# Kernel optimization log

Measured on AMD Instinct MI355X. Metric: run time of the kernel, lower is better.

## Reference

```python
import jax, jax.numpy as jnp
import numpy as np

C = 256
CK = C // 8  # qk projection dim


def setup_inputs() -> dict:
    key = jax.random.key(0)
    ks = jax.random.split(key, 8)
    B, H, W = 4, 64, 64
    x = jax.random.normal(ks[0], (B, C, W, H), dtype=jnp.float32)
    s = 1.0 / np.sqrt(C)
    Wf = jax.random.normal(ks[1], (CK, C), dtype=jnp.float32) * s
    bf = jax.random.normal(ks[2], (CK,), dtype=jnp.float32) * 0.01
    Wg = jax.random.normal(ks[3], (CK, C), dtype=jnp.float32) * s
    bg = jax.random.normal(ks[4], (CK,), dtype=jnp.float32) * 0.01
    Wh = jax.random.normal(ks[5], (C, C), dtype=jnp.float32) * s
    bh = jax.random.normal(ks[6], (C,), dtype=jnp.float32) * 0.01
    gamma = jax.random.normal(ks[7], (1,), dtype=jnp.float32) * 0.1
    return {"x": x, "Wf": Wf, "bf": bf, "Wg": Wg, "bg": bg,
            "Wh": Wh, "bh": bh, "gamma": gamma}


def reference(x, Wf, bf, Wg, bg, Wh, bh, gamma):
    B, Cc, Wd, Hd = x.shape
    N = Wd * Hd
    xf = x.reshape(B, Cc, N)  # B C N
    # 1x1 conv1d == channel matmul
    f = jnp.einsum('oc,bcn->bon', Wf, xf) + bf[None, :, None]  # B CK N
    g = jnp.einsum('oc,bcn->bon', Wg, xf) + bg[None, :, None]  # B CK N
    h = jnp.einsum('oc,bcn->bon', Wh, xf) + bh[None, :, None]  # B C N
    # s[b,i,j] = sum_k f[b,k,i] g[b,k,j]
    s = jnp.einsum('bki,bkj->bij', f, g)  # B N N
    attention = jax.nn.softmax(s, axis=-1)
    # out[b,c,i] = sum_j h[b,c,j] attention[b,i,j]
    out = jnp.einsum('bcj,bij->bci', h, attention)  # B C N
    out = out.reshape(B, Cc, Wd, Hd)
    return gamma[0] * out + x
```

## Files before the change

### kernel.cpp

```cpp
#include <hip/hip_runtime.h>

typedef __bf16 bf16x8 __attribute__((ext_vector_type(8)));
typedef __bf16 bf16x4 __attribute__((ext_vector_type(4)));
typedef float f32x4 __attribute__((ext_vector_type(4)));
typedef float f32x16 __attribute__((ext_vector_type(16)));

__device__ __forceinline__ f32x4 mfma16(bf16x8 a, bf16x8 b, f32x4 c) {
  return __builtin_amdgcn_mfma_f32_16x16x32_bf16(a, b, c, 0, 0, 0);
}
__device__ __forceinline__ f32x16 mfma32(bf16x8 a, bf16x8 b, f32x16 c) {
  return __builtin_amdgcn_mfma_f32_32x32x16_bf16(a, b, c, 0, 0, 0);
}

__device__ __forceinline__ unsigned int cvtpk(float a, float b) {
  union { __bf16 h[2]; unsigned int u; } r;
  r.h[0] = (__bf16)a; r.h[1] = (__bf16)b;
  return r.u;
}
__device__ __forceinline__ void swap32(unsigned int &a, unsigned int &b) {
  asm("v_permlane32_swap_b32 %0, %1" : "+v"(a), "+v"(b));
}

__global__ void wcvt_kernel(const float* __restrict__ Wf, const float* __restrict__ Wg,
                            const float* __restrict__ Wh, __bf16* __restrict__ Wb) {
  int i = blockIdx.x * 256 + threadIdx.x;
  float v;
  if (i < 8192)       v = Wf[i];
  else if (i < 16384) v = Wg[i - 8192];
  else                v = Wh[i - 16384];
  Wb[i] = (__bf16)v;
}

__global__ __launch_bounds__(512) void proj_kernel(
    const float* __restrict__ x, const float* __restrict__ bfv,
    const float* __restrict__ bgv, const float* __restrict__ bhv,
    const __bf16* __restrict__ Wb, __bf16* __restrict__ qkpk,
    __bf16* __restrict__ vpk) {
  __shared__ __align__(16) char smem[2560 + 18432];
  __bf16* xT = (__bf16*)smem;
  __bf16* ho = (__bf16*)(smem + 2560);

  const int t = threadIdx.x;
  const int l = t & 63, wg = t >> 6, q = l >> 4, l15 = l & 15;
  const int nh = wg & 1, oh = wg >> 1;
  const int bi = blockIdx.x;
  const int b = bi >> 7;
  const int nt = bi & 127;
  const int n0 = nt << 5;

  const float* xb = x + (size_t)b * 256 * 4096;

  f32x4 acc[5];
#pragma unroll
  for (int i = 0; i < 5; i++) acc[i] = (f32x4){0.f, 0.f, 0.f, 0.f};

  const int c_rel = t >> 4;
  const int n2 = (t & 15) * 2;

#pragma unroll 1
  for (int kc = 0; kc < 8; kc++) {
    __syncthreads();
    float2 v = *(const float2*)(xb + (size_t)(kc * 32 + c_rel) * 4096 + n0 + n2);
    xT[(n2 + 0) * 40 + c_rel] = (__bf16)v.x;
    xT[(n2 + 1) * 40 + c_rel] = (__bf16)v.y;
    __syncthreads();
    bf16x8 af = *(const bf16x8*)(xT + (nh * 16 + l15) * 40 + q * 8);
    const __bf16* wp = Wb + (size_t)(oh * 80 + l15) * 256 + kc * 32 + q * 8;
#pragma unroll
    for (int ot = 0; ot < 5; ot++) {
      bf16x8 bfr = *(const bf16x8*)(wp + (size_t)ot * 16 * 256);
      acc[ot] = mfma16(af, bfr, acc[ot]);
    }
  }

#pragma unroll
  for (int ot = 0; ot < 5; ot++) {
    int o = oh * 80 + ot * 16 + l15;
    float bias = (o < 32) ? bfv[o] : (o < 64) ? bgv[o - 32] : bhv[o - 64];
    if (oh == 0 && ot < 4) {
      int qk = o >> 5, fr = (o >> 4) & 1, hh = (o >> 3) & 1, e = o & 7;
      size_t base = ((size_t)b * 128 + nt) * 2048 + qk * 1024 + fr * 512 + hh * 256;
#pragma unroll
      for (int r = 0; r < 4; r++) {
        int n_rel = nh * 16 + q * 4 + r;
        qkpk[base + n_rel * 8 + e] = (__bf16)(acc[ot][r] + bias);
      }
    } else {
#pragma unroll
      for (int r = 0; r < 4; r++) {
        int n_rel = nh * 16 + q * 4 + r;
        ho[(o - 64) * 36 + n_rel] = (__bf16)(acc[ot][r] + bias);
      }
    }
  }
  __syncthreads();
  unsigned short* vpku = (unsigned short*)vpk + (size_t)b * 1048576;
  const unsigned short* hou = (const unsigned short*)ho;
  for (int e = t; e < 4096; e += 512) {
    int c = e >> 4, nn = (e & 15) * 2;
    int n = n0 + nn;
    int jc = n >> 4, hh = (n >> 3) & 1, ee = n & 7;
    unsigned int vv = *(const unsigned int*)(hou + c * 36 + nn);
    *(unsigned int*)(vpku + (((size_t)(jc * 2 + hh) * 256 + c) * 8 + ee)) = vv;
  }
}

__global__ __launch_bounds__(512, 2) void attn_kernel(
    const __bf16* __restrict__ qkpk, const __bf16* __restrict__ vpk,
    __bf16* __restrict__ pO, float* __restrict__ Lp) {
  __shared__ __align__(16) char smem[139264];

  const int t = threadIdx.x;
  const int l = t & 63, w = t >> 6;
  const int h = l >> 5, l31 = l & 31;

  const int bi = blockIdx.x;
  const int xcd = bi & 7;
  const int combo = xcd * 2 + ((bi >> 3) & 1);
  const int ig = bi >> 4;
  const int b = combo >> 2, jp = combo & 3;
  const int ti = ig * 8 + w;
  const int n0 = ti << 5;

  const __bf16* qkb = qkpk + (size_t)b * 262144;
  const __bf16* vpb = vpk + (size_t)b * 1048576;
  const int jq0 = jp << 10;

  const __bf16* qp = qkb + (size_t)ti * 2048 + h * 256 + l31 * 8;
  const bf16x8 qf0 = *(const bf16x8*)(qp);
  const bf16x8 qf1 = *(const bf16x8*)(qp + 512);

  f32x16 acc[8] = {};
  float rsum = 0.f;

  const __bf16* kbase = qkb + 1024 + h * 256 + l31 * 8;
  const int vlane = h * 2048 + l31 * 8;

  bf16x8 kf0 = *(const bf16x8*)(kbase + (size_t)(jq0 >> 5) * 2048);
  bf16x8 kf1 = *(const bf16x8*)(kbase + (size_t)(jq0 >> 5) * 2048 + 512);

#pragma unroll 1
  for (int ch = 0; ch < 32; ++ch) {
    f32x16 s = {};
    s = mfma32(kf0, qf0, s);
    s = mfma32(kf1, qf1, s);

    if (ch < 31) {
      const __bf16* kp = kbase + (size_t)((jq0 >> 5) + ch + 1) * 2048;
      kf0 = *(const bf16x8*)(kp);
      kf1 = *(const bf16x8*)(kp + 512);
    }

    const __bf16* vchunk = vpb + (size_t)((jq0 >> 4) + ch * 2) * 4096 + vlane;
    bf16x8 vb0[8];
#pragma unroll
    for (int ct = 0; ct < 8; ct++)
      vb0[ct] = *(const bf16x8*)(vchunk + ct * 256);

    float p[16];
#pragma unroll
    for (int r = 0; r < 16; r++) { p[r] = __expf(s[r]); rsum += p[r]; }

    unsigned int u0 = cvtpk(p[0], p[1]), v0 = cvtpk(p[2], p[3]);
    unsigned int w0 = cvtpk(p[4], p[5]), z0 = cvtpk(p[6], p[7]);
    swap32(u0, w0); swap32(v0, z0);
    unsigned int u1 = cvtpk(p[8], p[9]), v1 = cvtpk(p[10], p[11]);
    unsigned int w1 = cvtpk(p[12], p[13]), z1 = cvtpk(p[14], p[15]);
    swap32(u1, w1); swap32(v1, z1);
    union { unsigned int u[4]; bf16x8 v; } A0, A1;
    A0.u[0] = u0; A0.u[1] = v0; A0.u[2] = w0; A0.u[3] = z0;
    A1.u[0] = u1; A1.u[1] = v1; A1.u[2] = w1; A1.u[3] = z1;

    bf16x8 vb1[8];
#pragma unroll
    for (int ct = 0; ct < 8; ct++)
      vb1[ct] = *(const bf16x8*)(vchunk + 4096 + ct * 256);

#pragma unroll
    for (int ct = 0; ct < 8; ct++) acc[ct] = mfma32(A0.v, vb0[ct], acc[ct]);
#pragma unroll
    for (int ct = 0; ct < 8; ct++) acc[ct] = mfma32(A1.v, vb1[ct], acc[ct]);
  }

  __bf16* stage = (__bf16*)smem + (size_t)w * 8704;
#pragma unroll
  for (int ct = 0; ct < 8; ct++) {
    int c0 = ct * 32 + l31;
#pragma unroll
    for (int r = 0; r < 16; r++) {
      int i_loc = (r & 3) + 8 * (r >> 2) + 4 * h;
      stage[c0 * 34 + i_loc] = (__bf16)acc[ct][r];
    }
  }
  asm volatile("s_waitcnt lgkmcnt(0)" ::: "memory");

  unsigned short* ob = (unsigned short*)pO + (size_t)(jp * 4 + b) * 1048576 + n0;
  const unsigned short* su = (const unsigned short*)stage;
#pragma unroll 1
  for (int e = l; e < 4096; e += 64) {
    int c = e >> 4, i2 = (e & 15) * 2;
    unsigned int vv = *(const unsigned int*)(su + c * 34 + i2);
    *(unsigned int*)(ob + (size_t)c * 4096 + i2) = vv;
  }

  rsum += __shfl_xor(rsum, 32);
  if (l < 32) Lp[(size_t)(jp * 4 + b) * 4096 + n0 + l] = rsum;
}

__global__ __launch_bounds__(256) void norm_kernel(
    const float* __restrict__ x, const float* __restrict__ gamma_p,
    const __bf16* __restrict__ pO, const float* __restrict__ Lp,
    float* __restrict__ out) {
  const int bc = blockIdx.x;
  const int b = bc >> 8;
  const float gm = gamma_p[0];
  const float* xr = x + (size_t)bc * 4096;
  float* orow = out + (size_t)bc * 4096;
  const __bf16* pbase = pO + (size_t)bc * 4096;
  const float* lbase = Lp + (size_t)b * 4096;

  for (int i0 = threadIdx.x * 4; i0 < 4096; i0 += 1024) {
    float4 xv = *(const float4*)(xr + i0);
    float s0 = 0.f, s1 = 0.f, s2 = 0.f, s3 = 0.f;
    float l0 = 0.f, l1 = 0.f, l2 = 0.f, l3 = 0.f;
#pragma unroll
    for (int jp = 0; jp < 4; jp++) {
      bf16x4 pv = *(const bf16x4*)(pbase + (size_t)jp * 4194304 + i0);
      s0 += (float)pv[0]; s1 += (float)pv[1]; s2 += (float)pv[2]; s3 += (float)pv[3];
      float4 lv = *(const float4*)(lbase + (size_t)jp * 16384 + i0);
      l0 += lv.x; l1 += lv.y; l2 += lv.z; l3 += lv.w;
    }
    float4 ov;
    ov.x = gm * s0 / l0 + xv.x;
    ov.y = gm * s1 / l1 + xv.y;
    ov.z = gm * s2 / l2 + xv.z;
    ov.w = gm * s3 / l3 + xv.w;
    *(float4*)(orow + i0) = ov;
  }
}

extern "C" void kernel_launch(void* const* d_in, const int* in_sizes, int n_in,
                              void* d_out, int out_size, void* d_ws, size_t ws_size,
                              hipStream_t stream) {
  const float* x   = (const float*)d_in[0];
  const float* Wf  = (const float*)d_in[1];
  const float* bfv = (const float*)d_in[2];
  const float* Wg  = (const float*)d_in[3];
  const float* bgv = (const float*)d_in[4];
  const float* Wh  = (const float*)d_in[5];
  const float* bhv = (const float*)d_in[6];
  const float* gm  = (const float*)d_in[7];
  float* out = (float*)d_out;

  char* ws = (char*)d_ws;
  __bf16* Wb   = (__bf16*)ws;
  __bf16* qkpk = (__bf16*)(ws + 262144);
  __bf16* vpk  = (__bf16*)(ws + 2359296);
  __bf16* pO   = (__bf16*)(ws + 10747904);
  float*  Lp   = (float*)(ws + 44302336);

  hipLaunchKernelGGL(wcvt_kernel, dim3(320), dim3(256), 0, stream, Wf, Wg, Wh, Wb);
  hipLaunchKernelGGL(proj_kernel, dim3(512), dim3(512), 0, stream,
                     x, bfv, bgv, bhv, Wb, qkpk, vpk);
  hipLaunchKernelGGL(attn_kernel, dim3(256), dim3(512), 0, stream,
                     qkpk, vpk, pO, Lp);
  hipLaunchKernelGGL(norm_kernel, dim3(1024), dim3(256), 0, stream,
                     x, gm, pO, Lp, out);
}
```

Before: 162.0 us.

## Stage V chunks through double-buffered LDS shared by all waves

All 8 waves in a block read the same V chunk. Before, each wave loaded those 16 fragments from global memory itself. Now the block loads each chunk cooperatively (two 16-byte loads per thread) one iteration ahead, writes it into a double-buffered LDS region, and every wave reads its fragments from LDS. This cuts redundant global/L2 traffic by about 8x, at the cost of a block-wide barrier every iteration, which can serialize the waves and reduce latency hiding.

```diff
diff --git a/kernel.cpp b/kernel.cpp
--- a/kernel.cpp
+++ b/kernel.cpp
@@ -19,6 +19,11 @@
 }
 __device__ __forceinline__ void swap32(unsigned int &a, unsigned int &b) {
   asm("v_permlane32_swap_b32 %0, %1" : "+v"(a), "+v"(b));
+}
+
+__device__ __forceinline__ void sync_lds() {
+  asm volatile("s_waitcnt lgkmcnt(0)" ::: "memory");
+  __builtin_amdgcn_s_barrier();
 }
 
 __global__ void wcvt_kernel(const float* __restrict__ Wf, const float* __restrict__ Wg,
@@ -109,6 +114,7 @@
     const __bf16* __restrict__ qkpk, const __bf16* __restrict__ vpk,
     __bf16* __restrict__ pO, float* __restrict__ Lp) {
   __shared__ __align__(16) char smem[139264];
+  __bf16* Vbuf = (__bf16*)smem;
 
   const int t = threadIdx.x;
   const int l = t & 63, w = t >> 6;
@@ -134,13 +140,29 @@
   float rsum = 0.f;
 
   const __bf16* kbase = qkb + 1024 + h * 256 + l31 * 8;
-  const int vlane = h * 2048 + l31 * 8;
+  const int vfo = h * 2048 + l31 * 8;
 
   bf16x8 kf0 = *(const bf16x8*)(kbase + (size_t)(jq0 >> 5) * 2048);
   bf16x8 kf1 = *(const bf16x8*)(kbase + (size_t)(jq0 >> 5) * 2048 + 512);
 
+  {
+    const __bf16* src = vpb + (size_t)(jq0 >> 4) * 4096;
+    bf16x8 a = *(const bf16x8*)(src + t * 8);
+    bf16x8 c = *(const bf16x8*)(src + 4096 + t * 8);
+    *(bf16x8*)(Vbuf + t * 8) = a;
+    *(bf16x8*)(Vbuf + 4096 + t * 8) = c;
+  }
+  sync_lds();
+
 #pragma unroll 1
   for (int ch = 0; ch < 32; ++ch) {
+    bf16x8 sv0, sv1;
+    if (ch < 31) {
+      const __bf16* src = vpb + (size_t)((jq0 >> 4) + (ch + 1) * 2) * 4096;
+      sv0 = *(const bf16x8*)(src + t * 8);
+      sv1 = *(const bf16x8*)(src + 4096 + t * 8);
+    }
+
     f32x16 s = {};
     s = mfma32(kf0, qf0, s);
     s = mfma32(kf1, qf1, s);
@@ -150,12 +172,6 @@
       kf0 = *(const bf16x8*)(kp);
       kf1 = *(const bf16x8*)(kp + 512);
     }
-
-    const __bf16* vchunk = vpb + (size_t)((jq0 >> 4) + ch * 2) * 4096 + vlane;
-    bf16x8 vb0[8];
-#pragma unroll
-    for (int ct = 0; ct < 8; ct++)
-      vb0[ct] = *(const bf16x8*)(vchunk + ct * 256);
 
     float p[16];
 #pragma unroll
@@ -171,15 +187,24 @@
     A0.u[0] = u0; A0.u[1] = v0; A0.u[2] = w0; A0.u[3] = z0;
     A1.u[0] = u1; A1.u[1] = v1; A1.u[2] = w1; A1.u[3] = z1;
 
-    bf16x8 vb1[8];
-#pragma unroll
-    for (int ct = 0; ct < 8; ct++)
-      vb1[ct] = *(const bf16x8*)(vchunk + 4096 + ct * 256);
-
-#pragma unroll
-    for (int ct = 0; ct < 8; ct++) acc[ct] = mfma32(A0.v, vb0[ct], acc[ct]);
-#pragma unroll
-    for (int ct = 0; ct < 8; ct++) acc[ct] = mfma32(A1.v, vb1[ct], acc[ct]);
+    const __bf16* rb = Vbuf + (ch & 1) * 8192;
+#pragma unroll
+    for (int ct = 0; ct < 8; ct++) {
+      bf16x8 vv = *(const bf16x8*)(rb + vfo + ct * 256);
+      acc[ct] = mfma32(A0.v, vv, acc[ct]);
+    }
+#pragma unroll
+    for (int ct = 0; ct < 8; ct++) {
+      bf16x8 vv = *(const bf16x8*)(rb + 4096 + vfo + ct * 256);
+      acc[ct] = mfma32(A1.v, vv, acc[ct]);
+    }
+
+    if (ch < 31) {
+      __bf16* wb = Vbuf + ((ch + 1) & 1) * 8192;
+      *(bf16x8*)(wb + t * 8) = sv0;
+      *(bf16x8*)(wb + 4096 + t * 8) = sv1;
+    }
+    sync_lds();
   }
 
   __bf16* stage = (__bf16*)smem + (size_t)w * 8704;
```

After: 161.0 us. About the same (-0.6%).

## Split attention work per wave into 64 rows by 128 channels; fold log2e into K

Applied to the files above, without the earlier changes.

Each wave now handles two 32-row query tiles over half of the 256 value channels, where before it handled one query tile over all channels. Each V fragment loaded from global memory is therefore reused by two query tiles, which halves V traffic per unit of work, and V loads are software-pipelined across channel tiles. The K projection is prescaled by log2(e) so the softmax can use exp2 directly. In exchange, each wave now recomputes the QK scores for both tiles (the two channel-half waves duplicate that work), the staging buffer layout changes, and register pressure rises.

```diff
diff --git a/kernel.cpp b/kernel.cpp
--- a/kernel.cpp
+++ b/kernel.cpp
@@ -80,10 +80,11 @@
     if (oh == 0 && ot < 4) {
       int qk = o >> 5, fr = (o >> 4) & 1, hh = (o >> 3) & 1, e = o & 7;
       size_t base = ((size_t)b * 128 + nt) * 2048 + qk * 1024 + fr * 512 + hh * 256;
+      float sc = (o >= 32) ? 1.44269504089f : 1.0f;
 #pragma unroll
       for (int r = 0; r < 4; r++) {
         int n_rel = nh * 16 + q * 4 + r;
-        qkpk[base + n_rel * 8 + e] = (__bf16)(acc[ot][r] + bias);
+        qkpk[base + n_rel * 8 + e] = (__bf16)((acc[ot][r] + bias) * sc);
       }
     } else {
 #pragma unroll
@@ -108,7 +109,7 @@
 __global__ __launch_bounds__(512, 2) void attn_kernel(
     const __bf16* __restrict__ qkpk, const __bf16* __restrict__ vpk,
     __bf16* __restrict__ pO, float* __restrict__ Lp) {
-  __shared__ __align__(16) char smem[139264];
+  __shared__ __align__(16) char smem[135168];
 
   const int t = threadIdx.x;
   const int l = t & 63, w = t >> 6;
@@ -119,92 +120,121 @@
   const int combo = xcd * 2 + ((bi >> 3) & 1);
   const int ig = bi >> 4;
   const int b = combo >> 2, jp = combo & 3;
-  const int ti = ig * 8 + w;
-  const int n0 = ti << 5;
+  const int ih = w >> 1, chalf = w & 1;
+  const int i0 = ig * 256 + ih * 64;
 
   const __bf16* qkb = qkpk + (size_t)b * 262144;
   const __bf16* vpb = vpk + (size_t)b * 1048576;
   const int jq0 = jp << 10;
 
-  const __bf16* qp = qkb + (size_t)ti * 2048 + h * 256 + l31 * 8;
-  const bf16x8 qf0 = *(const bf16x8*)(qp);
-  const bf16x8 qf1 = *(const bf16x8*)(qp + 512);
-
-  f32x16 acc[8] = {};
-  float rsum = 0.f;
+  const __bf16* qpA = qkb + (size_t)(i0 >> 5) * 2048 + h * 256 + l31 * 8;
+  const bf16x8 qA0 = *(const bf16x8*)(qpA);
+  const bf16x8 qA1 = *(const bf16x8*)(qpA + 512);
+  const bf16x8 qB0 = *(const bf16x8*)(qpA + 2048);
+  const bf16x8 qB1 = *(const bf16x8*)(qpA + 2048 + 512);
+
+  f32x16 acc[2][4] = {};
+  float rsA = 0.f, rsB = 0.f;
 
   const __bf16* kbase = qkb + 1024 + h * 256 + l31 * 8;
-  const int vlane = h * 2048 + l31 * 8;
+  const int vfo = h * 2048 + (chalf * 128 + l31) * 8;
 
   bf16x8 kf0 = *(const bf16x8*)(kbase + (size_t)(jq0 >> 5) * 2048);
   bf16x8 kf1 = *(const bf16x8*)(kbase + (size_t)(jq0 >> 5) * 2048 + 512);
 
 #pragma unroll 1
   for (int ch = 0; ch < 32; ++ch) {
+    const __bf16* vchunk = vpb + (size_t)((jq0 >> 4) + ch * 2) * 4096 + vfo;
+    bf16x8 va = *(const bf16x8*)(vchunk);
+    bf16x8 vb_ = *(const bf16x8*)(vchunk + 4096);
+
     f32x16 s = {};
-    s = mfma32(kf0, qf0, s);
-    s = mfma32(kf1, qf1, s);
-
+    s = mfma32(kf0, qA0, s);
+    s = mfma32(kf1, qA1, s);
+    f32x16 sB = {};
+    sB = mfma32(kf0, qB0, sB);
+    sB = mfma32(kf1, qB1, sB);
+
+    bf16x8 kn0, kn1;
     if (ch < 31) {
       const __bf16* kp = kbase + (size_t)((jq0 >> 5) + ch + 1) * 2048;
-      kf0 = *(const bf16x8*)(kp);
-      kf1 = *(const bf16x8*)(kp + 512);
-    }
-
-    const __bf16* vchunk = vpb + (size_t)((jq0 >> 4) + ch * 2) * 4096 + vlane;
-    bf16x8 vb0[8];
-#pragma unroll
-    for (int ct = 0; ct < 8; ct++)
-      vb0[ct] = *(const bf16x8*)(vchunk + ct * 256);
+      kn0 = *(const bf16x8*)(kp);
+      kn1 = *(const bf16x8*)(kp + 512);
+    }
 
     float p[16];
 #pragma unroll
-    for (int r = 0; r < 16; r++) { p[r] = __expf(s[r]); rsum += p[r]; }
-
-    unsigned int u0 = cvtpk(p[0], p[1]), v0 = cvtpk(p[2], p[3]);
-    unsigned int w0 = cvtpk(p[4], p[5]), z0 = cvtpk(p[6], p[7]);
-    swap32(u0, w0); swap32(v0, z0);
-    unsigned int u1 = cvtpk(p[8], p[9]), v1 = cvtpk(p[10], p[11]);
-    unsigned int w1 = cvtpk(p[12], p[13]), z1 = cvtpk(p[14], p[15]);
-    swap32(u1, w1); swap32(v1, z1);
+    for (int r = 0; r < 16; r++) { p[r] = exp2f(s[r]); rsA += p[r]; }
+    unsigned int a0 = cvtpk(p[0], p[1]), a1 = cvtpk(p[2], p[3]);
+    unsigned int a2 = cvtpk(p[4], p[5]), a3 = cvtpk(p[6], p[7]);
+    swap32(a0, a2); swap32(a1, a3);
+    unsigned int a4 = cvtpk(p[8], p[9]), a5 = cvtpk(p[10], p[11]);
+    unsigned int a6 = cvtpk(p[12], p[13]), a7 = cvtpk(p[14], p[15]);
+    swap32(a4, a6); swap32(a5, a7);
     union { unsigned int u[4]; bf16x8 v; } A0, A1;
-    A0.u[0] = u0; A0.u[1] = v0; A0.u[2] = w0; A0.u[3] = z0;
-    A1.u[0] = u1; A1.u[1] = v1; A1.u[2] = w1; A1.u[3] = z1;
-
-    bf16x8 vb1[8];
-#pragma unroll
-    for (int ct = 0; ct < 8; ct++)
-      vb1[ct] = *(const bf16x8*)(vchunk + 4096 + ct * 256);
-
-#pragma unroll
-    for (int ct = 0; ct < 8; ct++) acc[ct] = mfma32(A0.v, vb0[ct], acc[ct]);
-#pragma unroll
-    for (int ct = 0; ct < 8; ct++) acc[ct] = mfma32(A1.v, vb1[ct], acc[ct]);
-  }
-
-  __bf16* stage = (__bf16*)smem + (size_t)w * 8704;
-#pragma unroll
-  for (int ct = 0; ct < 8; ct++) {
-    int c0 = ct * 32 + l31;
-#pragma unroll
-    for (int r = 0; r < 16; r++) {
-      int i_loc = (r & 3) + 8 * (r >> 2) + 4 * h;
-      stage[c0 * 34 + i_loc] = (__bf16)acc[ct][r];
-    }
-  }
+    A0.u[0] = a0; A0.u[1] = a1; A0.u[2] = a2; A0.u[3] = a3;
+    A1.u[0] = a4; A1.u[1] = a5; A1.u[2] = a6; A1.u[3] = a7;
+
+#pragma unroll
+    for (int r = 0; r < 16; r++) { p[r] = exp2f(sB[r]); rsB += p[r]; }
+    unsigned int b0 = cvtpk(p[0], p[1]), b1 = cvtpk(p[2], p[3]);
+    unsigned int b2 = cvtpk(p[4], p[5]), b3 = cvtpk(p[6], p[7]);
+    swap32(b0, b2); swap32(b1, b3);
+    unsigned int b4 = cvtpk(p[8], p[9]), b5 = cvtpk(p[10], p[11]);
+    unsigned int b6 = cvtpk(p[12], p[13]), b7 = cvtpk(p[14], p[15]);
+    swap32(b4, b6); swap32(b5, b7);
+    union { unsigned int u[4]; bf16x8 v; } B0, B1;
+    B0.u[0] = b0; B0.u[1] = b1; B0.u[2] = b2; B0.u[3] = b3;
+    B1.u[0] = b4; B1.u[1] = b5; B1.u[2] = b6; B1.u[3] = b7;
+
+    if (ch < 31) { kf0 = kn0; kf1 = kn1; }
+
+#pragma unroll
+    for (int ct = 0; ct < 4; ct++) {
+      bf16x8 na, nb;
+      if (ct < 3) {
+        na = *(const bf16x8*)(vchunk + (ct + 1) * 256);
+        nb = *(const bf16x8*)(vchunk + 4096 + (ct + 1) * 256);
+      }
+      acc[0][ct] = mfma32(A0.v, va, acc[0][ct]);
+      acc[1][ct] = mfma32(B0.v, va, acc[1][ct]);
+      acc[0][ct] = mfma32(A1.v, vb_, acc[0][ct]);
+      acc[1][ct] = mfma32(B1.v, vb_, acc[1][ct]);
+      if (ct < 3) { va = na; vb_ = nb; }
+    }
+  }
+
+  __bf16* stage = (__bf16*)smem + (size_t)w * 8448;
+#pragma unroll
+  for (int it = 0; it < 2; it++)
+#pragma unroll
+    for (int ct = 0; ct < 4; ct++) {
+      int c0 = ct * 32 + l31;
+#pragma unroll
+      for (int r = 0; r < 16; r++) {
+        int i_loc = it * 32 + (r & 3) + 8 * (r >> 2) + 4 * h;
+        stage[c0 * 66 + i_loc] = (__bf16)acc[it][ct][r];
+      }
+    }
   asm volatile("s_waitcnt lgkmcnt(0)" ::: "memory");
 
-  unsigned short* ob = (unsigned short*)pO + (size_t)(jp * 4 + b) * 1048576 + n0;
+  unsigned short* ob = (unsigned short*)pO + (size_t)(jp * 4 + b) * 1048576 +
+                       (size_t)chalf * 128 * 4096 + i0;
   const unsigned short* su = (const unsigned short*)stage;
 #pragma unroll 1
   for (int e = l; e < 4096; e += 64) {
-    int c = e >> 4, i2 = (e & 15) * 2;
-    unsigned int vv = *(const unsigned int*)(su + c * 34 + i2);
+    int c = e >> 5, i2 = (e & 31) * 2;
+    unsigned int vv = *(const unsigned int*)(su + c * 66 + i2);
     *(unsigned int*)(ob + (size_t)c * 4096 + i2) = vv;
   }
 
-  rsum += __shfl_xor(rsum, 32);
-  if (l < 32) Lp[(size_t)(jp * 4 + b) * 4096 + n0 + l] = rsum;
+  float ra = rsA + __shfl_xor(rsA, 32);
+  float rb = rsB + __shfl_xor(rsB, 32);
+  if (chalf == 0 && l < 32) {
+    float* lpb = Lp + (size_t)(jp * 4 + b) * 4096 + i0;
+    lpb[l] = ra;
+    lpb[32 + l] = rb;
+  }
 }
 
 __global__ __launch_bounds__(256) void norm_kernel(
```

Result: slower. 178.1 us (+9.9%).
